# Optimization experiments

Hardware: AMD Instinct MI355X
Metric: run time of the kernel (lower is better)

The kernel has to match this reference:

```python
import jax, jax.numpy as jnp
import numpy as np

B, S, E, H = 4, 2048, 1024, 16
D = E // H  # head_dim = 64


def setup_inputs() -> dict:
    key = jax.random.key(0)
    ks = jax.random.split(key, 6)
    x = jax.random.normal(ks[0], (B, S, E), dtype=jnp.float32)
    # realistic padding: per-batch valid lengths in [S//2, S]
    lengths = jax.random.randint(ks[1], (B,), S // 2, S + 1)
    padding_mask = jnp.arange(S)[None, :] < lengths[:, None]  # [B,S] bool
    init = 1.0 / np.sqrt(E)
    qkv_w = jax.random.uniform(ks[2], (3 * E, E), jnp.float32, -init, init)
    qkv_b = jnp.zeros((3 * E,), jnp.float32)
    proj_w = jax.random.uniform(ks[3], (E, E), jnp.float32, -init, init)
    proj_b = jnp.zeros((E,), jnp.float32)
    return {"x": x, "padding_mask": padding_mask, "qkv_w": qkv_w,
            "qkv_b": qkv_b, "proj_w": proj_w, "proj_b": proj_b}


def reference(x, padding_mask, qkv_w, qkv_b, proj_w, proj_b):
    b, s, e = x.shape
    scale = D ** -0.5
    qkv = x @ qkv_w.T + qkv_b                      # [B,S,3E]
    qkv = qkv.reshape(b, s, 3, H, D).transpose(2, 0, 3, 1, 4)  # [3,B,H,S,D]
    q, k, v = qkv[0], qkv[1], qkv[2]
    attn = jnp.einsum('bhsd,bhtd->bhst', q, k) * scale         # [B,H,S,S]
    attn = jnp.where(padding_mask[:, None, None, :], attn, -jnp.inf)
    attn = jax.nn.softmax(attn, axis=-1)
    out = jnp.einsum('bhst,bhtd->bhsd', attn, v)               # [B,H,S,D]
    out = out.transpose(0, 2, 1, 3).reshape(b, s, e)           # [B,S,E]
    return out @ proj_w.T + proj_b
```

## Files before the change

kernel.cpp:

```cpp
#include <hip/hip_runtime.h>
#include <hip/hip_bf16.h>
#include <stdint.h>

#define S_LEN 2048
#define NB 4
#define NH 16
#define HD 64
#define E_DIM 1024

typedef __attribute__((ext_vector_type(8))) short s16x8;
typedef __attribute__((ext_vector_type(4))) float f32x4;
typedef __attribute__((ext_vector_type(16))) float f32x16;
typedef __attribute__((ext_vector_type(4))) int i32x4;

__device__ __forceinline__ short f2bf(float f) {
  union { float f; uint32_t u; } x; x.f = f;
  uint32_t r = (x.u + 0x7FFF + ((x.u >> 16) & 1)) >> 16;
  return (short)r;
}

__device__ __forceinline__ int cvtpk_bf16(float lo, float hi) {
  int r;
  asm("v_cvt_pk_bf16_f32 %0, %1, %2" : "=v"(r) : "v"(lo), "v"(hi));
  return r;
}

__device__ __forceinline__ void glds16(const void* g, void* l) {
  __builtin_amdgcn_global_load_lds(
      (const __attribute__((address_space(1))) unsigned int*)g,
      (__attribute__((address_space(3))) unsigned int*)l, 16, 0, 0);
}

__global__ void cvt_f32_bf16(const float* __restrict__ src, short* __restrict__ dst, int n4) {
  int i = blockIdx.x * blockDim.x + threadIdx.x;
  if (i < n4) {
    float4 v = reinterpret_cast<const float4*>(src)[i];
    short4 o;
    o.x = f2bf(v.x); o.y = f2bf(v.y); o.z = f2bf(v.z); o.w = f2bf(v.w);
    reinterpret_cast<short4*>(dst)[i] = o;
  }
}

__global__ void compute_lengths(const unsigned char* __restrict__ mask, int* __restrict__ lengths) {
  int b = blockIdx.x;
  unsigned char b0 = mask[0], b1 = mask[1];
  int mode = (b0 == 0) ? 2 : ((b1 != 0) ? 0 : 1);
  int cnt = 0;
  for (int s = threadIdx.x; s < S_LEN; s += blockDim.x) {
    bool v;
    if (mode == 0)      v = mask[(size_t)b * S_LEN + s] != 0;
    else if (mode == 1) v = reinterpret_cast<const int*>(mask)[(size_t)b * S_LEN + s] != 0;
    else                v = reinterpret_cast<const float*>(mask)[(size_t)b * S_LEN + s] != 0.f;
    cnt += v ? 1 : 0;
  }
  __shared__ int red[256];
  red[threadIdx.x] = cnt;
  __syncthreads();
  for (int o = 128; o > 0; o >>= 1) {
    if (threadIdx.x < o) red[threadIdx.x] += red[threadIdx.x + o];
    __syncthreads();
  }
  if (threadIdx.x == 0) lengths[b] = red[0];
}

template <int MODE>
__launch_bounds__(256, 3)
__global__ void gemm_nt(const short* __restrict__ A, const short* __restrict__ Bw,
                        const float* __restrict__ bias, float* __restrict__ Cout,
                        short* __restrict__ Qo, short* __restrict__ Ko, short* __restrict__ Vo,
                        int M, int N, int K) {
  __shared__ short Al[2][128 * 32];
  __shared__ short Bl[2][128 * 32];
  const int tid = threadIdx.x;
  const int lane = tid & 63;
  const int w = tid >> 6;
  const int wm = w >> 1, wn = w & 1;
  const int l15 = lane & 15, l4 = lane >> 4;
  const int bm = blockIdx.y, bn = blockIdx.x;

  const int srow = w * 32 + (lane >> 2);
  const int scol = (lane & 3) * 8;
  const short* Ag = A + (size_t)(bm * 128 + srow) * K + scol;
  const short* Bg = Bw + (size_t)(bn * 128 + srow) * K + scol;
  const size_t row16 = (size_t)16 * K;

  f32x4 acc[4][4];
#pragma unroll
  for (int i = 0; i < 4; ++i)
#pragma unroll
    for (int j = 0; j < 4; ++j) acc[i][j] = (f32x4){0.f, 0.f, 0.f, 0.f};

  auto stage = [&](int kt, int buf) {
    const short* a0 = Ag + kt * 32;
    const short* b0 = Bg + kt * 32;
    short* Asm = &Al[buf][(w * 32) * 32];
    short* Bsm = &Bl[buf][(w * 32) * 32];
    glds16(a0, Asm);
    glds16(a0 + row16, Asm + 16 * 32);
    glds16(b0, Bsm);
    glds16(b0 + row16, Bsm + 16 * 32);
  };

  const int NT = K / 32;
  stage(0, 0);
  __syncthreads();
  for (int kt = 0; kt < NT; ++kt) {
    const int cur = kt & 1;
    if (kt + 1 < NT) stage(kt + 1, cur ^ 1);
    s16x8 af[4], bf[4];
#pragma unroll
    for (int mi = 0; mi < 4; ++mi)
      af[mi] = *reinterpret_cast<const s16x8*>(&Al[cur][(wm * 64 + mi * 16 + l15) * 32 + l4 * 8]);
#pragma unroll
    for (int nj = 0; nj < 4; ++nj)
      bf[nj] = *reinterpret_cast<const s16x8*>(&Bl[cur][(wn * 64 + nj * 16 + l15) * 32 + l4 * 8]);
#pragma unroll
    for (int mi = 0; mi < 4; ++mi)
#pragma unroll
      for (int nj = 0; nj < 4; ++nj)
        acc[mi][nj] = __builtin_amdgcn_mfma_f32_16x16x32_bf16(af[mi], bf[nj], acc[mi][nj], 0, 0, 0);
    __syncthreads();
  }

#pragma unroll
  for (int mi = 0; mi < 4; ++mi) {
#pragma unroll
    for (int nj = 0; nj < 4; ++nj) {
      const int m0 = bm * 128 + wm * 64 + mi * 16 + l4 * 4;
      const int n = bn * 128 + wn * 64 + nj * 16 + l15;
      const float bv = bias[n];
      if (MODE == 0) {
#pragma unroll
        for (int r = 0; r < 4; ++r)
          Cout[(size_t)(m0 + r) * N + n] = acc[mi][nj][r] + bv;
      } else {
        const int which = n >> 10, e = n & 1023, h = e >> 6, d = e & 63;
        const int b = m0 >> 11, s = m0 & 2047;
        const size_t bh = (size_t)(b * NH + h);
        if (which == 2) {
          short4 pk;
          pk.x = f2bf(acc[mi][nj][0] + bv); pk.y = f2bf(acc[mi][nj][1] + bv);
          pk.z = f2bf(acc[mi][nj][2] + bv); pk.w = f2bf(acc[mi][nj][3] + bv);
          *reinterpret_cast<short4*>(&Vo[(bh * HD + d) * S_LEN + s]) = pk;
        } else if (which == 0) {
#pragma unroll
          for (int r = 0; r < 4; ++r)
            Qo[(bh * S_LEN + s + r) * HD + d] = f2bf((acc[mi][nj][r] + bv) * 0.180336880111f);
        } else {
#pragma unroll
          for (int r = 0; r < 4; ++r)
            Ko[(bh * S_LEN + s + r) * HD + d] = f2bf(acc[mi][nj][r] + bv);
        }
      }
    }
  }
}

__launch_bounds__(256, 3)
__global__ void attn_fwd(const short* __restrict__ Q, const short* __restrict__ K,
                         const short* __restrict__ Vt, short* __restrict__ ctx,
                         const int* __restrict__ lengths) {
  __shared__ short Kl[2][64 * 64];
  __shared__ short Vl[2][64 * 64];
  const int tid = threadIdx.x;
  const int lane = tid & 63, w = tid >> 6;
  const int l31 = lane & 31, hi = lane >> 5;
  const int bid = blockIdx.x;
  const int xcd = bid & 7, idx = bid >> 3;
  const int bh = xcd * 8 + (idx >> 4);
  const int qt = idx & 15;
  const int b = bh >> 4;
  const int len = lengths[b];

  const size_t bhS = (size_t)bh * S_LEN;
  const int qrow = qt * 128 + w * 32 + l31;
  const short* Qb = Q + (bhS + qrow) * HD + hi * 8;
  s16x8 qf0 = *reinterpret_cast<const s16x8*>(Qb);
  s16x8 qf1 = *reinterpret_cast<const s16x8*>(Qb + 16);
  s16x8 qf2 = *reinterpret_cast<const s16x8*>(Qb + 32);
  s16x8 qf3 = *reinterpret_cast<const s16x8*>(Qb + 48);

  const int rr = lane >> 3, bb = lane & 7;
  const int swz = (bb ^ rr) << 4;
  const char* KgB = (const char*)(K + bhS * HD);
  const char* VgB = (const char*)(Vt + bhS * HD);
  const int krow0 = 16 * w + rr;
  const size_t koff0 = (size_t)krow0 * 128 + swz;
  const size_t koff1 = (size_t)(krow0 + 8) * 128 + swz;
  const size_t voff0 = (size_t)krow0 * (S_LEN * 2) + swz;
  const size_t voff1 = (size_t)(krow0 + 8) * (S_LEN * 2) + swz;

  auto stage = [&](int kt, int buf) {
    const char* ks = KgB + (size_t)kt * (64 * 128);
    const char* vs = VgB + (size_t)kt * 128;
    short* kd = &Kl[buf][w * 1024];
    short* vd = &Vl[buf][w * 1024];
    glds16(ks + koff0, kd);
    glds16(ks + koff1, kd + 512);
    glds16(vs + voff0, vd);
    glds16(vs + voff1, vd + 512);
  };

  f32x16 o0, o1;
#pragma unroll
  for (int r = 0; r < 16; ++r) { o0[r] = 0.f; o1[r] = 0.f; }
  float m_run = -3e38f, l_run = 0.f;

  const int sw = (l31 & 7) << 4;

  auto tile_body = [&](int kt, int buf) {
    const char* kb = (const char*)&Kl[buf][0];
    const char* vb = (const char*)&Vl[buf][0];
    f32x16 sa0, sa1;
#pragma unroll
    for (int r = 0; r < 16; ++r) { sa0[r] = 0.f; sa1[r] = 0.f; }
    __builtin_amdgcn_s_setprio(1);
#pragma unroll
    for (int n = 0; n < 4; ++n) {
      s16x8 kf = *reinterpret_cast<const s16x8*>(kb + l31 * 128 + ((n * 32 + hi * 16) ^ sw));
      const s16x8 q = (n == 0) ? qf0 : (n == 1) ? qf1 : (n == 2) ? qf2 : qf3;
      sa0 = __builtin_amdgcn_mfma_f32_32x32x16_bf16(kf, q, sa0, 0, 0, 0);
    }
#pragma unroll
    for (int n = 0; n < 4; ++n) {
      s16x8 kf = *reinterpret_cast<const s16x8*>(kb + (32 + l31) * 128 + ((n * 32 + hi * 16) ^ sw));
      const s16x8 q = (n == 0) ? qf0 : (n == 1) ? qf1 : (n == 2) ? qf2 : qf3;
      sa1 = __builtin_amdgcn_mfma_f32_32x32x16_bf16(kf, q, sa1, 0, 0, 0);
    }
    __builtin_amdgcn_s_setprio(0);
    const int mrem = len - kt * 64;
    if (mrem < 64) {
#pragma unroll
      for (int r = 0; r < 16; ++r) {
        int off = (r & 3) + 8 * (r >> 2) + 4 * hi;
        if (off >= mrem) sa0[r] = -3e38f;
        if (off + 32 >= mrem) sa1[r] = -3e38f;
      }
    }
    float mx = fmaxf(sa0[0], sa1[0]);
#pragma unroll
    for (int r = 1; r < 16; ++r) mx = fmaxf(mx, fmaxf(sa0[r], sa1[r]));
    mx = fmaxf(mx, __shfl_xor(mx, 32));
    if (!__all(mx <= m_run + 8.f)) {
      float mnew = fmaxf(m_run, mx);
      float al = exp2f(m_run - mnew);
#pragma unroll
      for (int r = 0; r < 16; ++r) { o0[r] *= al; o1[r] *= al; }
      l_run *= al;
      m_run = mnew;
    }
    float ssum = 0.f;
#pragma unroll
    for (int r = 0; r < 16; ++r) {
      sa0[r] = exp2f(sa0[r] - m_run);
      sa1[r] = exp2f(sa1[r] - m_run);
      ssum += sa0[r] + sa1[r];
    }
    l_run += ssum + __shfl_xor(ssum, 32);
    union { i32x4 i; s16x8 h; } uf[4];
#pragma unroll
    for (int sub = 0; sub < 2; ++sub) {
      const f32x16& sa = sub ? sa1 : sa0;
      int A0 = cvtpk_bf16(sa[0], sa[1]),   B0 = cvtpk_bf16(sa[2], sa[3]);
      int A1 = cvtpk_bf16(sa[4], sa[5]),   B1 = cvtpk_bf16(sa[6], sa[7]);
      int A2 = cvtpk_bf16(sa[8], sa[9]),   B2 = cvtpk_bf16(sa[10], sa[11]);
      int A3 = cvtpk_bf16(sa[12], sa[13]), B3 = cvtpk_bf16(sa[14], sa[15]);
      int sA0 = __shfl_xor(A0, 32), sB0 = __shfl_xor(B0, 32);
      int sA1 = __shfl_xor(A1, 32), sB1 = __shfl_xor(B1, 32);
      int sA2 = __shfl_xor(A2, 32), sB2 = __shfl_xor(B2, 32);
      int sA3 = __shfl_xor(A3, 32), sB3 = __shfl_xor(B3, 32);
      uf[sub * 2 + 0].i = hi ? (i32x4){sA1, sB1, A1, B1} : (i32x4){A0, B0, sA0, sB0};
      uf[sub * 2 + 1].i = hi ? (i32x4){sA3, sB3, A3, B3} : (i32x4){A2, B2, sA2, sB2};
    }
    __builtin_amdgcn_s_setprio(1);
#pragma unroll
    for (int kc = 0; kc < 4; ++kc) {
      s16x8 v0 = *reinterpret_cast<const s16x8*>(vb + l31 * 128 + ((kc * 32 + hi * 16) ^ sw));
      o0 = __builtin_amdgcn_mfma_f32_32x32x16_bf16(v0, uf[kc].h, o0, 0, 0, 0);
    }
#pragma unroll
    for (int kc = 0; kc < 4; ++kc) {
      s16x8 v1 = *reinterpret_cast<const s16x8*>(vb + (32 + l31) * 128 + ((kc * 32 + hi * 16) ^ sw));
      o1 = __builtin_amdgcn_mfma_f32_32x32x16_bf16(v1, uf[kc].h, o1, 0, 0, 0);
    }
    __builtin_amdgcn_s_setprio(0);
  };

  const int ntt = (len + 63) >> 6;
  stage(0, 0);
  __syncthreads();
  for (int kt = 0; kt < ntt; ++kt) {
    const int buf = kt & 1;
    if (kt + 1 < ntt) stage(kt + 1, buf ^ 1);
    tile_body(kt, buf);
    __syncthreads();
  }

  const float inv = 1.f / l_run;
  const int h = bh & 15;
  const size_t base = ((size_t)b * S_LEN + qrow) * E_DIM + h * HD + 4 * hi;
#pragma unroll
  for (int rq = 0; rq < 4; ++rq) {
    short4 a, c;
    a.x = f2bf(o0[4 * rq + 0] * inv); a.y = f2bf(o0[4 * rq + 1] * inv);
    a.z = f2bf(o0[4 * rq + 2] * inv); a.w = f2bf(o0[4 * rq + 3] * inv);
    *reinterpret_cast<short4*>(&ctx[base + 8 * rq]) = a;
    c.x = f2bf(o1[4 * rq + 0] * inv); c.y = f2bf(o1[4 * rq + 1] * inv);
    c.z = f2bf(o1[4 * rq + 2] * inv); c.w = f2bf(o1[4 * rq + 3] * inv);
    *reinterpret_cast<short4*>(&ctx[base + 32 + 8 * rq]) = c;
  }
}

extern "C" void kernel_launch(void* const* d_in, const int* in_sizes, int n_in,
                              void* d_out, int out_size, void* d_ws, size_t ws_size,
                              hipStream_t stream) {
  const float* x = (const float*)d_in[0];
  const unsigned char* mask = (const unsigned char*)d_in[1];
  const float* qkv_w = (const float*)d_in[2];
  const float* qkv_b = (const float*)d_in[3];
  const float* proj_w = (const float*)d_in[4];
  const float* proj_b = (const float*)d_in[5];
  float* out = (float*)d_out;

  const size_t SZ_X = (size_t)NB * S_LEN * E_DIM;
  short* xb = (short*)d_ws;
  short* wqb = xb + SZ_X;
  short* wpb = wqb + (size_t)3 * E_DIM * E_DIM;
  short* Qs = wpb + (size_t)E_DIM * E_DIM;
  short* Ks = Qs + SZ_X;
  short* Vts = Ks + SZ_X;
  short* ctx = Vts + SZ_X;
  int* lens = (int*)(ctx + SZ_X);

  cvt_f32_bf16<<<(int)(SZ_X / 4 / 256), 256, 0, stream>>>(x, xb, (int)(SZ_X / 4));
  cvt_f32_bf16<<<3 * E_DIM * E_DIM / 4 / 256, 256, 0, stream>>>(qkv_w, wqb, 3 * E_DIM * E_DIM / 4);
  cvt_f32_bf16<<<E_DIM * E_DIM / 4 / 256, 256, 0, stream>>>(proj_w, wpb, E_DIM * E_DIM / 4);
  compute_lengths<<<NB, 256, 0, stream>>>(mask, lens);

  dim3 g1(3 * E_DIM / 128, NB * S_LEN / 128);
  gemm_nt<1><<<g1, 256, 0, stream>>>(xb, wqb, qkv_b, nullptr, Qs, Ks, Vts,
                                     NB * S_LEN, 3 * E_DIM, E_DIM);

  attn_fwd<<<NB * NH * (S_LEN / 128), 256, 0, stream>>>(Qs, Ks, Vts, ctx, lens);

  dim3 g2(E_DIM / 128, NB * S_LEN / 128);
  gemm_nt<0><<<g2, 256, 0, stream>>>(ctx, wpb, proj_b, out, nullptr, nullptr, nullptr,
                                     NB * S_LEN, E_DIM, E_DIM);
}
```

Measured before the change: 345.7 us.

## Use permlane32 swaps in attention softmax and remap block IDs across XCDs

Replaces the __shfl_xor(…,32) cross-half exchanges in the attention softmax (row max, row sum and the bf16 P-fragment repacking) with v_permlane32_swap, which avoids LDS-routed bpermute traffic and the per-lane select. The max reduction is reorganised into a tree of 3-input max operations to shorten the dependency chain. The GEMM block index is remapped so that consecutive blocks on each XCD cover contiguous tiles, and the attention grid mapping is changed so each XCD handles interleaved heads with q-tiles grouped. The GEMM remap hardcodes 64 row tiles and assumes the grid size is divisible by 8, so it is only correct for the shapes used here.

```diff
diff --git a/kernel.cpp b/kernel.cpp
--- a/kernel.cpp
+++ b/kernel.cpp
@@ -12,6 +12,7 @@
 typedef __attribute__((ext_vector_type(4))) float f32x4;
 typedef __attribute__((ext_vector_type(16))) float f32x16;
 typedef __attribute__((ext_vector_type(4))) int i32x4;
+typedef __attribute__((ext_vector_type(2))) unsigned u32x2;
 
 __device__ __forceinline__ short f2bf(float f) {
   union { float f; uint32_t u; } x; x.f = f;
@@ -23,6 +24,21 @@
   int r;
   asm("v_cvt_pk_bf16_f32 %0, %1, %2" : "=v"(r) : "v"(lo), "v"(hi));
   return r;
+}
+
+__device__ __forceinline__ u32x2 pl32(unsigned a, unsigned b) {
+  auto r = __builtin_amdgcn_permlane32_swap(a, b, false, false);
+  return (u32x2){(unsigned)r[0], (unsigned)r[1]};
+}
+__device__ __forceinline__ float pl32_max(float v) {
+  unsigned u = __builtin_bit_cast(unsigned, v);
+  u32x2 r = pl32(u, u);
+  return fmaxf(__builtin_bit_cast(float, r[0]), __builtin_bit_cast(float, r[1]));
+}
+__device__ __forceinline__ float pl32_sum(float v) {
+  unsigned u = __builtin_bit_cast(unsigned, v);
+  u32x2 r = pl32(u, u);
+  return __builtin_bit_cast(float, r[0]) + __builtin_bit_cast(float, r[1]);
 }
 
 __device__ __forceinline__ void glds16(const void* g, void* l) {
@@ -76,7 +92,11 @@
   const int w = tid >> 6;
   const int wm = w >> 1, wn = w & 1;
   const int l15 = lane & 15, l4 = lane >> 4;
-  const int bm = blockIdx.y, bn = blockIdx.x;
+  const int flat = blockIdx.y * gridDim.x + blockIdx.x;
+  const int cpx = (gridDim.x * gridDim.y) >> 3;
+  const int nf = (flat & 7) * cpx + (flat >> 3);
+  const int bm = nf & 63;
+  const int bn = nf >> 6;
 
   const int srow = w * 32 + (lane >> 2);
   const int scol = (lane & 3) * 8;
@@ -167,8 +187,8 @@
   const int l31 = lane & 31, hi = lane >> 5;
   const int bid = blockIdx.x;
   const int xcd = bid & 7, idx = bid >> 3;
-  const int bh = xcd * 8 + (idx >> 4);
-  const int qt = idx & 15;
+  const int sub = idx & 7, qt = idx >> 3;
+  const int bh = sub * 8 + xcd;
   const int b = bh >> 4;
   const int len = lengths[b];
 
@@ -237,10 +257,22 @@
         if (off + 32 >= mrem) sa1[r] = -3e38f;
       }
     }
-    float mx = fmaxf(sa0[0], sa1[0]);
-#pragma unroll
-    for (int r = 1; r < 16; ++r) mx = fmaxf(mx, fmaxf(sa0[r], sa1[r]));
-    mx = fmaxf(mx, __shfl_xor(mx, 32));
+    float a0 = fmaxf(fmaxf(sa0[0], sa0[1]), sa0[2]);
+    float a1 = fmaxf(fmaxf(sa0[3], sa0[4]), sa0[5]);
+    float a2 = fmaxf(fmaxf(sa0[6], sa0[7]), sa0[8]);
+    float a3 = fmaxf(fmaxf(sa0[9], sa0[10]), sa0[11]);
+    float a4 = fmaxf(fmaxf(sa0[12], sa0[13]), sa0[14]);
+    float a5 = fmaxf(fmaxf(sa0[15], sa1[0]), sa1[1]);
+    float a6 = fmaxf(fmaxf(sa1[2], sa1[3]), sa1[4]);
+    float a7 = fmaxf(fmaxf(sa1[5], sa1[6]), sa1[7]);
+    float a8 = fmaxf(fmaxf(sa1[8], sa1[9]), sa1[10]);
+    float a9 = fmaxf(fmaxf(sa1[11], sa1[12]), sa1[13]);
+    float aa = fmaxf(sa1[14], sa1[15]);
+    a0 = fmaxf(fmaxf(a0, a1), a2);
+    a3 = fmaxf(fmaxf(a3, a4), a5);
+    a6 = fmaxf(fmaxf(a6, a7), a8);
+    a9 = fmaxf(a9, aa);
+    float mx = pl32_max(fmaxf(fmaxf(a0, a3), fmaxf(a6, a9)));
     if (!__all(mx <= m_run + 8.f)) {
       float mnew = fmaxf(m_run, mx);
       float al = exp2f(m_run - mnew);
@@ -249,28 +281,29 @@
       l_run *= al;
       m_run = mnew;
     }
-    float ssum = 0.f;
+    float s0 = 0.f, s1 = 0.f;
 #pragma unroll
     for (int r = 0; r < 16; ++r) {
       sa0[r] = exp2f(sa0[r] - m_run);
       sa1[r] = exp2f(sa1[r] - m_run);
-      ssum += sa0[r] + sa1[r];
-    }
-    l_run += ssum + __shfl_xor(ssum, 32);
+      s0 += sa0[r];
+      s1 += sa1[r];
+    }
+    l_run += pl32_sum(s0 + s1);
     union { i32x4 i; s16x8 h; } uf[4];
 #pragma unroll
-    for (int sub = 0; sub < 2; ++sub) {
-      const f32x16& sa = sub ? sa1 : sa0;
-      int A0 = cvtpk_bf16(sa[0], sa[1]),   B0 = cvtpk_bf16(sa[2], sa[3]);
-      int A1 = cvtpk_bf16(sa[4], sa[5]),   B1 = cvtpk_bf16(sa[6], sa[7]);
-      int A2 = cvtpk_bf16(sa[8], sa[9]),   B2 = cvtpk_bf16(sa[10], sa[11]);
-      int A3 = cvtpk_bf16(sa[12], sa[13]), B3 = cvtpk_bf16(sa[14], sa[15]);
-      int sA0 = __shfl_xor(A0, 32), sB0 = __shfl_xor(B0, 32);
-      int sA1 = __shfl_xor(A1, 32), sB1 = __shfl_xor(B1, 32);
-      int sA2 = __shfl_xor(A2, 32), sB2 = __shfl_xor(B2, 32);
-      int sA3 = __shfl_xor(A3, 32), sB3 = __shfl_xor(B3, 32);
-      uf[sub * 2 + 0].i = hi ? (i32x4){sA1, sB1, A1, B1} : (i32x4){A0, B0, sA0, sB0};
-      uf[sub * 2 + 1].i = hi ? (i32x4){sA3, sB3, A3, B3} : (i32x4){A2, B2, sA2, sB2};
+    for (int sb = 0; sb < 2; ++sb) {
+      const f32x16& sa = sb ? sa1 : sa0;
+      unsigned A0 = cvtpk_bf16(sa[0], sa[1]),   B0 = cvtpk_bf16(sa[2], sa[3]);
+      unsigned A1 = cvtpk_bf16(sa[4], sa[5]),   B1 = cvtpk_bf16(sa[6], sa[7]);
+      unsigned A2 = cvtpk_bf16(sa[8], sa[9]),   B2 = cvtpk_bf16(sa[10], sa[11]);
+      unsigned A3 = cvtpk_bf16(sa[12], sa[13]), B3 = cvtpk_bf16(sa[14], sa[15]);
+      u32x2 rA01 = pl32(A0, A1);
+      u32x2 rB01 = pl32(B0, B1);
+      u32x2 rA23 = pl32(A2, A3);
+      u32x2 rB23 = pl32(B2, B3);
+      uf[sb * 2 + 0].i = (i32x4){(int)rA01[0], (int)rB01[0], (int)rA01[1], (int)rB01[1]};
+      uf[sb * 2 + 1].i = (i32x4){(int)rA23[0], (int)rB23[0], (int)rA23[1], (int)rB23[1]};
     }
     __builtin_amdgcn_s_setprio(1);
 #pragma unroll
```

New measurement: 332.0 us. -4.0%, faster.
